# Kernel optimization log

Hardware: AMD Instinct MI355X
Metric: run time of the kernel (lower is better)

The kernel has to match this reference:

```python
import jax, jax.numpy as jnp
import numpy as np

D = 1024
H = 16
HD = D // H
DFF = 4 * D
B, L = 2, 2048
EPS = 1e-5


def setup_inputs() -> dict:
    key = jax.random.key(0)
    ks = jax.random.split(key, 12)
    s = lambda fan_in: 1.0 / np.sqrt(fan_in)
    inp = {
        "x": jax.random.normal(ks[0], (B, L, D), jnp.float32),
        "mask": jnp.ones((1, 1, L, L), jnp.bool_),
        "ln_g": jnp.ones((D,), jnp.float32),
        "ln_b": jnp.zeros((D,), jnp.float32),
        "qkv_w": jax.random.uniform(ks[1], (3 * D, D), jnp.float32, -s(D), s(D)),
        "qkv_b": jax.random.uniform(ks[2], (3 * D,), jnp.float32, -s(D), s(D)),
        "wo_w": jax.random.uniform(ks[3], (D, D), jnp.float32, -s(D), s(D)),
        "wo_b": jax.random.uniform(ks[4], (D,), jnp.float32, -s(D), s(D)),
        "m0_w": jax.random.uniform(ks[5], (DFF, D), jnp.float32, -s(D), s(D)),
        "m0_b": jax.random.uniform(ks[6], (DFF,), jnp.float32, -s(D), s(D)),
        "m1_w": jax.random.uniform(ks[7], (D, DFF), jnp.float32, -s(DFF), s(DFF)),
        "m1_b": jax.random.uniform(ks[8], (D,), jnp.float32, -s(DFF), s(DFF)),
    }
    return inp


def _layer_norm(x, g, b):
    mu = jnp.mean(x, axis=-1, keepdims=True)
    var = jnp.var(x, axis=-1, keepdims=True)
    return (x - mu) * jax.lax.rsqrt(var + EPS) * g + b


def reference(x, mask, ln_g, ln_b, qkv_w, qkv_b, wo_w, wo_b, m0_w, m0_b, m1_w, m1_b):
    b, l, d = x.shape
    # --- pre-norm self-attention ---
    xn = _layer_norm(x, ln_g, ln_b)
    qkv = xn @ qkv_w.T + qkv_b                       # [B, L, 3D]
    qkv = qkv.reshape(b, l, 3, H, HD).transpose(2, 0, 3, 1, 4)  # [3, B, H, L, HD]
    q, k, v = qkv[0], qkv[1], qkv[2]
    scores = jnp.einsum("bhld,bhmd->bhlm", q, k) / np.sqrt(HD)  # [B, H, L, L]
    scores = jnp.where(mask, scores, -1e9)
    attn = jax.nn.softmax(scores, axis=-1)
    ctx = jnp.einsum("bhlm,bhmd->bhld", attn, v)     # [B, H, L, HD]
    ctx = ctx.transpose(0, 2, 1, 3).reshape(b, l, d)
    x = x + ctx @ wo_w.T + wo_b
    # --- GELU MLP (same shared LayerNorm params) ---
    xn = _layer_norm(x, ln_g, ln_b)
    h = jax.nn.gelu(xn @ m0_w.T + m0_b, approximate=False)
    return x + h @ m1_w.T + m1_b
```

## Files before the change

kernel.cpp:

```cpp
#include <hip/hip_runtime.h>
#include <hip/hip_bf16.h>
#include <hip/hip_cooperative_groups.h>
#include <math.h>

#define BL 4096
#define DM 1024
#define NH 16
#define HD 64
#define DFF 4096
#define SEQ 2048
#define EPS 1e-5f
#define QSCALE 0.18033688011112042f

typedef __bf16 bf16x8 __attribute__((ext_vector_type(8)));
typedef float f32x4 __attribute__((ext_vector_type(4)));
typedef float f32x16 __attribute__((ext_vector_type(16)));

__device__ __forceinline__ unsigned short f2bf(float f) {
    __hip_bfloat16 h = __float2bfloat16(f);
    return *reinterpret_cast<unsigned short*>(&h);
}

__device__ __forceinline__ unsigned int pack2bf(float p0, float p1) {
    unsigned int u0 = __builtin_bit_cast(unsigned int, p0) + 0x8000u;
    unsigned int u1 = __builtin_bit_cast(unsigned int, p1) + 0x8000u;
    return __builtin_amdgcn_perm(u1, u0, 0x07060302);
}

__device__ __forceinline__ void gload_lds16(const void* g, void* l) {
    __builtin_amdgcn_global_load_lds(
        (const __attribute__((address_space(1))) unsigned int*)g,
        (__attribute__((address_space(3))) unsigned int*)l,
        16, 0, 0);
}

__global__ __launch_bounds__(256)
void prep_kernel(const float* __restrict__ x, const float* __restrict__ g,
                 const float* __restrict__ b, unsigned short* __restrict__ o,
                 const float* __restrict__ s0, const float* __restrict__ s1,
                 const float* __restrict__ s2, const float* __restrict__ s3,
                 unsigned short* __restrict__ d0, unsigned short* __restrict__ d1,
                 unsigned short* __restrict__ d2, unsigned short* __restrict__ d3,
                 int n0, int n1, int n2, int n3) {
    const int bid = blockIdx.x;
    const int tid = threadIdx.x;
    if (bid >= BL) {
        int i = (bid - BL) * 256 + tid;
        const float* s; unsigned short* d; int j = i;
        if (j < n0) { s = s0; d = d0; }
        else if ((j -= n0) < n1) { s = s1; d = d1; }
        else if ((j -= n1) < n2) { s = s2; d = d2; }
        else if ((j -= n2) < n3) { s = s3; d = d3; }
        else return;
        float4 v = ((const float4*)s)[j];
        ushort4 ov = {f2bf(v.x), f2bf(v.y), f2bf(v.z), f2bf(v.w)};
        ((ushort4*)d)[j] = ov;
        return;
    }
    const int row = bid;
    const float* xr = x + (size_t)row * DM;
    float4 v = *(const float4*)(xr + tid * 4);
    float s_  = v.x + v.y + v.z + v.w;
    float ss = v.x*v.x + v.y*v.y + v.z*v.z + v.w*v.w;
    #pragma unroll
    for (int off = 32; off > 0; off >>= 1) {
        s_ += __shfl_down(s_, off);
        ss += __shfl_down(ss, off);
    }
    __shared__ float ps[4], pss[4];
    __shared__ float sh_mu, sh_rs;
    int wid = tid >> 6, lane = tid & 63;
    if (lane == 0) { ps[wid] = s_; pss[wid] = ss; }
    __syncthreads();
    if (tid == 0) {
        float S = ps[0] + ps[1] + ps[2] + ps[3];
        float SS = pss[0] + pss[1] + pss[2] + pss[3];
        float mu = S * (1.0f / DM);
        float var = SS * (1.0f / DM) - mu * mu;
        sh_mu = mu;
        sh_rs = 1.0f / sqrtf(var + EPS);
    }
    __syncthreads();
    float mu = sh_mu, rs = sh_rs;
    float4 gv = *(const float4*)(g + tid * 4);
    float4 bv = *(const float4*)(b + tid * 4);
    ushort4 ov;
    ov.x = f2bf((v.x - mu) * rs * gv.x + bv.x);
    ov.y = f2bf((v.y - mu) * rs * gv.y + bv.y);
    ov.z = f2bf((v.z - mu) * rs * gv.z + bv.z);
    ov.w = f2bf((v.w - mu) * rs * gv.w + bv.w);
    *(ushort4*)(o + (size_t)row * DM + tid * 4) = ov;
}

template <int EPI, typename OUT_T>
__global__ __launch_bounds__(256)
void gemm_bt_mfma(const unsigned short* __restrict__ A,
                  const unsigned short* __restrict__ B,
                  const float* __restrict__ bias, const float* __restrict__ res,
                  OUT_T* __restrict__ C, int M, int N, int K,
                  unsigned short* __restrict__ vt) {
    __shared__ unsigned short smem[2][16384];
    const int tid = threadIdx.x, lane = tid & 63, wave = tid >> 6;

    const int id   = blockIdx.x;
    const int xcd  = id & 7, slot = id >> 3;
    const int R    = (M / 128) >> 3;
    const int by   = xcd * R + (slot % R);
    const int bx   = slot / R;
    const int m0 = by * 128, n0 = bx * 128;
    const int wm = (wave >> 1) * 64, wn = (wave & 1) * 64;
    const int srow = lane >> 3, sslot = lane & 7;
    const int fr = lane & 15, g = lane >> 4;

    f32x4 acc[4][4] = {};

    auto stage = [&](int b, int kt) {
        unsigned short* As = smem[b];
        unsigned short* Bs = smem[b] + 8192;
        #pragma unroll
        for (int rep = 0; rep < 8; rep++) {
            const int c = rep * 4 + wave;
            const bool isA = (c < 16);
            const int cc = isA ? c : c - 16;
            const int cr = cc * 8 + srow;
            const unsigned short* src = (isA ? A + (size_t)(m0 + cr) * K
                                             : B + (size_t)(n0 + cr) * K)
                                        + kt + ((sslot ^ (cr & 7)) * 8);
            gload_lds16(src, (char*)(isA ? As : Bs) + cc * 1024);
        }
    };

    stage(0, 0);
    const int NT = K >> 6;
    for (int ti = 0; ti < NT; ti++) {
        __syncthreads();
        if (ti + 1 < NT) stage((ti + 1) & 1, (ti + 1) * 64);
        const unsigned short* As = smem[ti & 1];
        const unsigned short* Bs = As + 8192;
        #pragma unroll
        for (int ko = 0; ko < 2; ko++) {
            const int col = (((ko * 4 + g) ^ (fr & 7)) * 8);
            bf16x8 af[4], bfv[4];
            #pragma unroll
            for (int i = 0; i < 4; i++)
                af[i] = *(const bf16x8*)(As + (wm + i * 16 + fr) * 64 + col);
            #pragma unroll
            for (int j = 0; j < 4; j++)
                bfv[j] = *(const bf16x8*)(Bs + (wn + j * 16 + fr) * 64 + col);
            #pragma unroll
            for (int i = 0; i < 4; i++)
                #pragma unroll
                for (int j = 0; j < 4; j++)
                    acc[i][j] = __builtin_amdgcn_mfma_f32_16x16x32_bf16(af[i], bfv[j], acc[i][j], 0, 0, 0);
        }
    }

    const int col  = lane & 15;
    const int rowq = (lane >> 4) * 4;
    float bs[4];
    #pragma unroll
    for (int j = 0; j < 4; j++) bs[j] = bias[n0 + wn + j * 16 + col];

    if (EPI == 3 && n0 >= 2048) {
        __syncthreads();
        unsigned short* sc = smem[0];
        #pragma unroll
        for (int i = 0; i < 4; i++) {
            const int l0 = wm + i * 16 + rowq;
            #pragma unroll
            for (int j = 0; j < 4; j++) {
                const int dcol = wn + j * 16 + col;
                float v0 = acc[i][j][0] + bs[j], v1 = acc[i][j][1] + bs[j];
                float v2 = acc[i][j][2] + bs[j], v3 = acc[i][j][3] + bs[j];
                uint2 pk = {pack2bf(v0, v1), pack2bf(v2, v3)};
                char* p = (char*)sc + dcol * 256 +
                          (((l0 >> 3) ^ (dcol & 7)) * 16) + (l0 & 7) * 2;
                *(uint2*)p = pk;
            }
        }
        __syncthreads();
        const int bb = m0 >> 11, lbase = m0 & 2047;
        #pragma unroll
        for (int k = 0; k < 8; k++) {
            const int oid = tid + k * 256;
            const int dcol = oid >> 4, lc = oid & 15;
            uint4 val = *(const uint4*)((const char*)sc + dcol * 256 +
                                        ((lc ^ (dcol & 7)) * 16));
            const int c = n0 + dcol;
            const int d = c & 63, hh2 = (c >> 6) & 15;
            *(uint4*)(vt + ((size_t)((bb * 16 + hh2) * 64 + d)) * 2048 + lbase + lc * 8) = val;
        }
        return;
    }

    #pragma unroll
    for (int i = 0; i < 4; i++) {
        #pragma unroll
        for (int r = 0; r < 4; r++) {
            const size_t row = (size_t)(m0 + wm + i * 16 + rowq + r);
            #pragma unroll
            for (int j = 0; j < 4; j++) {
                const int c = n0 + wn + j * 16 + col;
                const size_t off = row * N + c;
                float v = acc[i][j][r] + bs[j];
                if (EPI == 1) v += res[off];
                if (EPI == 2) {
                    float u = v * (0.7978845608028654f + 0.035677408136300125f * v * v);
                    float e = __builtin_amdgcn_exp2f(u * 2.885390081777927f);
                    float th = 1.0f - 2.0f * __builtin_amdgcn_rcpf(e + 1.0f);
                    v = 0.5f * v * (1.0f + th);
                }
                if (EPI == 3) {
                    float vq = (c < 1024) ? v * QSCALE : v;
                    ((unsigned short*)C)[off] = f2bf(vq);
                } else if constexpr (sizeof(OUT_T) == 2) {
                    ((unsigned short*)C)[off] = f2bf(v);
                } else {
                    ((float*)C)[off] = v;
                }
            }
        }
    }
}

template <int K>
__global__ __launch_bounds__(512)
void gemm_splitk_res(const unsigned short* __restrict__ A,
                     const unsigned short* __restrict__ B,
                     const float* __restrict__ bias,
                     const float* __restrict__ res,
                     float* __restrict__ C) {
    __shared__ unsigned short smem[2][2][16384];
    const int id   = blockIdx.x;
    const int xcd  = id & 7, slot = id >> 3;
    const int by   = xcd * 4 + (slot & 3);
    const int bx   = slot >> 2;
    const int m0 = by * 128, n0 = bx * 128;
    const int tid = threadIdx.x, lane = tid & 63, wave = tid >> 6;
    const int grp = wave >> 2, w4 = wave & 3;
    const int wm = (w4 >> 1) * 64, wn = (w4 & 1) * 64;
    const int srow = lane >> 3, sslot = lane & 7;
    const int fr = lane & 15, g = lane >> 4;
    const int kg0 = grp * (K / 2);
    constexpr int NT = K / 128;

    f32x4 acc[4][4] = {};

    auto stage = [&](int b, int kt) {
        unsigned short* As = smem[grp][b];
        unsigned short* Bs = smem[grp][b] + 8192;
        #pragma unroll
        for (int rep = 0; rep < 8; rep++) {
            const int c = rep * 4 + w4;
            const bool isA = (c < 16);
            const int cc = isA ? c : c - 16;
            const int cr = cc * 8 + srow;
            const unsigned short* src = (isA ? A + (size_t)(m0 + cr) * K
                                             : B + (size_t)(n0 + cr) * K)
                                        + kt + ((sslot ^ (cr & 7)) * 8);
            gload_lds16(src, (char*)(isA ? As : Bs) + cc * 1024);
        }
    };

    stage(0, kg0);
    for (int ti = 0; ti < NT; ti++) {
        __syncthreads();
        if (ti + 1 < NT) stage((ti + 1) & 1, kg0 + (ti + 1) * 64);
        const unsigned short* As = smem[grp][ti & 1];
        const unsigned short* Bs = As + 8192;
        #pragma unroll
        for (int ko = 0; ko < 2; ko++) {
            const int col = (((ko * 4 + g) ^ (fr & 7)) * 8);
            bf16x8 af[4], bfv[4];
            #pragma unroll
            for (int i = 0; i < 4; i++)
                af[i] = *(const bf16x8*)(As + (wm + i * 16 + fr) * 64 + col);
            #pragma unroll
            for (int j = 0; j < 4; j++)
                bfv[j] = *(const bf16x8*)(Bs + (wn + j * 16 + fr) * 64 + col);
            #pragma unroll
            for (int i = 0; i < 4; i++)
                #pragma unroll
                for (int j = 0; j < 4; j++)
                    acc[i][j] = __builtin_amdgcn_mfma_f32_16x16x32_bf16(af[i], bfv[j], acc[i][j], 0, 0, 0);
        }
    }

    __syncthreads();
    float* ox = (float*)smem;
    if (grp == 1) {
        float* bp = ox + w4 * 4096;
        #pragma unroll
        for (int i = 0; i < 4; i++)
            #pragma unroll
            for (int j = 0; j < 4; j++)
                *(f32x4*)(bp + (i * 4 + j) * 256 + lane * 4) = acc[i][j];
    }
    __syncthreads();
    if (grp == 1) return;
    {
        float* bp = ox + w4 * 4096;
        #pragma unroll
        for (int i = 0; i < 4; i++)
            #pragma unroll
            for (int j = 0; j < 4; j++)
                acc[i][j] += *(const f32x4*)(bp + (i * 4 + j) * 256 + lane * 4);
    }

    const int col = lane & 15, rowq = (lane >> 4) * 4;
    float bs[4];
    #pragma unroll
    for (int j = 0; j < 4; j++) bs[j] = bias[n0 + wn + j * 16 + col];
    #pragma unroll
    for (int i = 0; i < 4; i++)
        #pragma unroll
        for (int r = 0; r < 4; r++) {
            const size_t row = (size_t)(m0 + wm + i * 16 + rowq + r);
            #pragma unroll
            for (int j = 0; j < 4; j++) {
                const int c = n0 + wn + j * 16 + col;
                const size_t off = row * 1024 + c;
                C[off] = acc[i][j][r] + bs[j] + res[off];
            }
        }
}

__global__ __launch_bounds__(512)
void fused_wo_ln(const unsigned short* __restrict__ A,
                 const unsigned short* __restrict__ B,
                 const float* __restrict__ bias,
                 const float* __restrict__ res,
                 float* __restrict__ C,
                 const float* __restrict__ gw,
                 const float* __restrict__ bw,
                 unsigned short* __restrict__ xn) {
    constexpr int K = 1024;
    __shared__ unsigned short smem[2][2][16384];
    const int id   = blockIdx.x;
    const int xcd  = id & 7, slot = id >> 3;
    const int by   = xcd * 4 + (slot & 3);
    const int bx   = slot >> 2;
    const int m0 = by * 128, n0 = bx * 128;
    const int tid = threadIdx.x, lane = tid & 63, wave = tid >> 6;
    const int grp = wave >> 2, w4 = wave & 3;
    const int wm = (w4 >> 1) * 64, wn = (w4 & 1) * 64;
    const int srow = lane >> 3, sslot = lane & 7;
    const int fr = lane & 15, g = lane >> 4;
    const int kg0 = grp * (K / 2);
    constexpr int NT = K / 128;

    f32x4 acc[4][4] = {};

    auto stage = [&](int b, int kt) {
        unsigned short* As = smem[grp][b];
        unsigned short* Bs = smem[grp][b] + 8192;
        #pragma unroll
        for (int rep = 0; rep < 8; rep++) {
            const int c = rep * 4 + w4;
            const bool isA = (c < 16);
            const int cc = isA ? c : c - 16;
            const int cr = cc * 8 + srow;
            const unsigned short* src = (isA ? A + (size_t)(m0 + cr) * K
                                             : B + (size_t)(n0 + cr) * K)
                                        + kt + ((sslot ^ (cr & 7)) * 8);
            gload_lds16(src, (char*)(isA ? As : Bs) + cc * 1024);
        }
    };

    stage(0, kg0);
    for (int ti = 0; ti < NT; ti++) {
        __syncthreads();
        if (ti + 1 < NT) stage((ti + 1) & 1, kg0 + (ti + 1) * 64);
        const unsigned short* As = smem[grp][ti & 1];
        const unsigned short* Bs = As + 8192;
        #pragma unroll
        for (int ko = 0; ko < 2; ko++) {
            const int col = (((ko * 4 + g) ^ (fr & 7)) * 8);
            bf16x8 af[4], bfv[4];
            #pragma unroll
            for (int i = 0; i < 4; i++)
                af[i] = *(const bf16x8*)(As + (wm + i * 16 + fr) * 64 + col);
            #pragma unroll
            for (int j = 0; j < 4; j++)
                bfv[j] = *(const bf16x8*)(Bs + (wn + j * 16 + fr) * 64 + col);
            #pragma unroll
            for (int i = 0; i < 4; i++)
                #pragma unroll
                for (int j = 0; j < 4; j++)
                    acc[i][j] = __builtin_amdgcn_mfma_f32_16x16x32_bf16(af[i], bfv[j], acc[i][j], 0, 0, 0);
        }
    }

    __syncthreads();
    float* ox = (float*)smem;
    if (grp == 1) {
        float* bp = ox + w4 * 4096;
        #pragma unroll
        for (int i = 0; i < 4; i++)
            #pragma unroll
            for (int j = 0; j < 4; j++)
                *(f32x4*)(bp + (i * 4 + j) * 256 + lane * 4) = acc[i][j];
    }
    __syncthreads();
    if (grp == 0) {
        float* bp = ox + w4 * 4096;
        #pragma unroll
        for (int i = 0; i < 4; i++)
            #pragma unroll
            for (int j = 0; j < 4; j++)
                acc[i][j] += *(const f32x4*)(bp + (i * 4 + j) * 256 + lane * 4);

        const int col = lane & 15, rowq = (lane >> 4) * 4;
        float bs[4];
        #pragma unroll
        for (int j = 0; j < 4; j++) bs[j] = bias[n0 + wn + j * 16 + col];
        #pragma unroll
        for (int i = 0; i < 4; i++)
            #pragma unroll
            for (int r = 0; r < 4; r++) {
                const size_t row = (size_t)(m0 + wm + i * 16 + rowq + r);
                #pragma unroll
                for (int j = 0; j < 4; j++) {
                    const int c = n0 + wn + j * 16 + col;
                    const size_t off = row * 1024 + c;
                    C[off] = acc[i][j][r] + bs[j] + res[off];
                }
            }
    }

    cooperative_groups::this_grid().sync();

    float* ph = (float*)smem;
    const int team = tid >> 8, tt = tid & 255;
    const int wl = (tid >> 6) & 3;
    for (int it = 0; it < 8; it++) {
        const int row = id * 16 + it * 2 + team;
        const float* xr = C + (size_t)row * DM;
        float4 v = *(const float4*)(xr + tt * 4);
        float s  = v.x + v.y + v.z + v.w;
        float ss = v.x*v.x + v.y*v.y + v.z*v.z + v.w*v.w;
        #pragma unroll
        for (int off = 32; off > 0; off >>= 1) {
            s  += __shfl_down(s, off);
            ss += __shfl_down(ss, off);
        }
        if ((tid & 63) == 0) { ph[team * 8 + wl] = s; ph[team * 8 + 4 + wl] = ss; }
        __syncthreads();
        float S  = ph[team*8+0] + ph[team*8+1] + ph[team*8+2] + ph[team*8+3];
        float SS = ph[team*8+4] + ph[team*8+5] + ph[team*8+6] + ph[team*8+7];
        float mu = S * (1.0f / DM);
        float var = SS * (1.0f / DM) - mu * mu;
        float rs = 1.0f / sqrtf(var + EPS);
        float4 gv = *(const float4*)(gw + tt * 4);
        float4 bv = *(const float4*)(bw + tt * 4);
        ushort4 ov;
        ov.x = f2bf((v.x - mu) * rs * gv.x + bv.x);
        ov.y = f2bf((v.y - mu) * rs * gv.y + bv.y);
        ov.z = f2bf((v.z - mu) * rs * gv.z + bv.z);
        ov.w = f2bf((v.w - mu) * rs * gv.w + bv.w);
        *(ushort4*)(xn + (size_t)row * DM + tt * 4) = ov;
        __syncthreads();
    }
}

__global__ __launch_bounds__(512)
void attn_mfma(const unsigned short* __restrict__ qkv,
               const unsigned short* __restrict__ vt,
               unsigned short* __restrict__ ctx) {
    __shared__ unsigned short smem[2][16384];
    const int bid = blockIdx.x;
    const int xcd = bid & 7, sl = bid >> 3;
    const int qt = sl & 15, pg = sl >> 4;
    const int pair = pg * 8 + xcd;
    const int h = pair & 15, b = pair >> 4;
    const int tid = threadIdx.x, lane = tid & 63, wave = tid >> 6;
    const int grp = wave >> 2, w4 = wave & 3;
    const int hh = lane >> 5, mm = lane & 31;
    const int q0 = b * 2048 + qt * 128 + w4 * 32;

    unsigned short* Ks = smem[grp];
    unsigned short* Vt = smem[grp] + 8192;

    bf16x8 qf[4];
    const unsigned short* qb = qkv + (size_t)(q0 + mm) * 3072 + h * 64 + hh * 8;
    #pragma unroll
    for (int s = 0; s < 4; s++) qf[s] = *(const bf16x8*)(qb + s * 16);

    const int skey = lane >> 3;
    const int sgr  = (lane & 7) ^ (skey & 7);
    const unsigned short* kbase = qkv + ((size_t)(b * 2048) + skey) * 3072 + 1024 + h * 64 + sgr * 8;
    const unsigned short* vbase = vt + ((size_t)((b * 16 + h) * 64) + skey) * 2048 + sgr * 8;

    float l_lane = 0.0f;
    f32x16 o_acc[2] = {};
    const int kt0 = grp * 1024;

    for (int ti = 0; ti < 8; ti++) {
        const int kt = kt0 + ti * 128;
        __syncthreads();
        #pragma unroll
        for (int rep = 0; rep < 4; rep++) {
            int c = rep * 4 + w4;
            gload_lds16(kbase + (size_t)(kt + c * 8) * 3072, (char*)Ks + c * 1024);
        }
        #pragma unroll
        for (int rep = 0; rep < 2; rep++) {
            int c = rep * 4 + w4;
            gload_lds16(vbase + (size_t)(c * 8) * 2048 + kt,      (char*)Vt + c * 1024);
            gload_lds16(vbase + (size_t)(c * 8) * 2048 + kt + 64, (char*)Vt + 8192 + c * 1024);
        }
        __syncthreads();

        #pragma unroll
        for (int sub = 0; sub < 2; sub++) {
            f32x16 sT[2] = {};
            __builtin_amdgcn_s_setprio(1);
            #pragma unroll
            for (int t = 0; t < 2; t++)
                #pragma unroll
                for (int s = 0; s < 4; s++) {
                    bf16x8 kf = *(const bf16x8*)(Ks + (sub * 64 + t * 32 + mm) * 64 + ((s * 2 + hh) ^ (mm & 7)) * 8);
                    sT[t] = __builtin_amdgcn_mfma_f32_32x32x16_bf16(kf, qf[s], sT[t], 0, 0, 0);
                }
            __builtin_amdgcn_s_setprio(0);

            unsigned int pk[2][8];
            #pragma unroll
            for (int t = 0; t < 2; t++)
                #pragma unroll
                for (int e = 0; e < 8; e++) {
                    float p0 = __builtin_amdgcn_exp2f(sT[t][2 * e]);
                    float p1 = __builtin_amdgcn_exp2f(sT[t][2 * e + 1]);
                    l_lane += p0 + p1;
                    pk[t][e] = pack2bf(p0, p1);
                }

            __builtin_amdgcn_s_setprio(1);
            #pragma unroll
            for (int w = 0; w < 4; w++) {
                const int t = w >> 1, eb = (w & 1) * 4;
                unsigned int a0 = pk[t][eb + 0], a1 = pk[t][eb + 1];
                unsigned int a2 = pk[t][eb + 2], a3 = pk[t][eb + 3];
                asm("v_permlane32_swap_b32 %0, %1" : "+v"(a0), "+v"(a2));
                asm("v_permlane32_swap_b32 %0, %1" : "+v"(a1), "+v"(a3));
                union { unsigned int u[4]; bf16x8 v; } af;
                af.u[0] = a0; af.u[1] = a1; af.u[2] = a2; af.u[3] = a3;
                #pragma unroll
                for (int dt = 0; dt < 2; dt++) {
                    bf16x8 vf = *(const bf16x8*)(Vt + sub * 4096 + (dt * 32 + mm) * 64 + ((w * 2 + hh) ^ (mm & 7)) * 8);
                    o_acc[dt] = __builtin_amdgcn_mfma_f32_32x32x16_bf16(af.v, vf, o_acc[dt], 0, 0, 0);
                }
            }
            __builtin_amdgcn_s_setprio(0);
        }
    }

    float l_red = l_lane + __shfl_xor(l_lane, 32);
    __syncthreads();
    float* ox = (float*)smem;
    float* lx = (float*)((char*)smem + 32768);
    if (grp == 1) {
        float* base = ox + w4 * 2048;
        #pragma unroll
        for (int dt = 0; dt < 2; dt++)
            #pragma unroll
            for (int r = 0; r < 16; r++)
                base[(dt * 16 + r) * 64 + lane] = o_acc[dt][r];
        if (hh == 0) lx[w4 * 32 + mm] = l_red;
    }
    __syncthreads();
    if (grp == 1) return;
    {
        float* base = ox + w4 * 2048;
        #pragma unroll
        for (int dt = 0; dt < 2; dt++)
            #pragma unroll
            for (int r = 0; r < 16; r++)
                o_acc[dt][r] += base[(dt * 16 + r) * 64 + lane];
        l_red += lx[w4 * 32 + mm];
    }

    float inv_own = 1.0f / l_red;
    #pragma unroll
    for (int r = 0; r < 16; r++) {
        const int rowq = (r & 3) + 8 * (r >> 2) + 4 * hh;
        float inv = __shfl(inv_own, rowq);
        size_t base = (size_t)(q0 + rowq) * 1024 + h * 64 + mm;
        ctx[base]      = f2bf(o_acc[0][r] * inv);
        ctx[base + 32] = f2bf(o_acc[1][r] * inv);
    }
}

extern "C" void kernel_launch(void* const* d_in, const int* in_sizes, int n_in,
                              void* d_out, int out_size, void* d_ws, size_t ws_size,
                              hipStream_t stream) {
    const float* x     = (const float*)d_in[0];
    const float* ln_g  = (const float*)d_in[2];
    const float* ln_b  = (const float*)d_in[3];
    const float* qkv_w = (const float*)d_in[4];
    const float* qkv_b = (const float*)d_in[5];
    const float* wo_w  = (const float*)d_in[6];
    const float* wo_b  = (const float*)d_in[7];
    const float* m0_w  = (const float*)d_in[8];
    const float* m0_b  = (const float*)d_in[9];
    const float* m1_w  = (const float*)d_in[10];
    const float* m1_b  = (const float*)d_in[11];
    float* out = (float*)d_out;

    char* ws = (char*)d_ws;
    unsigned short* xn_bf  = (unsigned short*)(ws);
    unsigned short* qkv_bf = (unsigned short*)(ws + (size_t)8  * 1024 * 1024);
    unsigned short* vt_bf  = (unsigned short*)(ws + (size_t)32 * 1024 * 1024);
    unsigned short* ctx_bf = (unsigned short*)(ws + (size_t)40 * 1024 * 1024);
    unsigned short* h_bf   = (unsigned short*)(ws + (size_t)48 * 1024 * 1024);
    unsigned short* qkvw_b = (unsigned short*)(ws + (size_t)80 * 1024 * 1024);
    unsigned short* wow_b  = (unsigned short*)(ws + (size_t)86 * 1024 * 1024);
    unsigned short* m0w_b  = (unsigned short*)(ws + (size_t)88 * 1024 * 1024);
    unsigned short* m1w_b  = (unsigned short*)(ws + (size_t)96 * 1024 * 1024);

    {
        int n0 = 3 * DM * DM / 4, n1 = DM * DM / 4, n2 = DFF * DM / 4, n3 = DM * DFF / 4;
        int tot = n0 + n1 + n2 + n3;
        prep_kernel<<<BL + (tot + 255) / 256, 256, 0, stream>>>(
            x, ln_g, ln_b, xn_bf,
            qkv_w, wo_w, m0_w, m1_w, qkvw_b, wow_b, m0w_b, m1w_b, n0, n1, n2, n3);
    }

    gemm_bt_mfma<3, unsigned short><<<(3072 / 128) * (BL / 128), 256, 0, stream>>>(
        xn_bf, qkvw_b, qkv_b, nullptr, qkv_bf, BL, 3072, DM, vt_bf);
    attn_mfma<<<2 * NH * (SEQ / 128), 512, 0, stream>>>(qkv_bf, vt_bf, ctx_bf);
    {
        void* args[] = {(void*)&ctx_bf, (void*)&wow_b, (void*)&wo_b, (void*)&x,
                        (void*)&out, (void*)&ln_g, (void*)&ln_b, (void*)&xn_bf};
        hipLaunchCooperativeKernel((void*)fused_wo_ln, dim3(256), dim3(512),
                                   args, 0, stream);
    }
    gemm_bt_mfma<2, unsigned short><<<(DFF / 128) * (BL / 128), 256, 0, stream>>>(
        xn_bf, m0w_b, m0_b, nullptr, h_bf, BL, DFF, DM, nullptr);
    gemm_splitk_res<4096><<<256, 512, 0, stream>>>(h_bf, m1w_b, m1_b, out, out);
}
```

Measured before the change: 379.0 us.

## Replace cooperative grid sync with per-row-block atomic counter for fused LayerNorm

Drops the cooperative launch and grid-wide barrier in the Wo GEMM plus LayerNorm kernel. Each 128-row block now increments a counter once its output tile is written, and the last of the 8 column tiles to finish runs LayerNorm on those 128 rows, one wave per row. This avoids the whole-grid wait and the cooperative launch overhead, at the cost of leaving the LayerNorm work on 32 blocks only. Counters are zeroed in the prep kernel, and a fallback path with a separate GEMM and LN kernel is used if the workspace is too small.

```diff
diff --git a/kernel.cpp b/kernel.cpp
--- a/kernel.cpp
+++ b/kernel.cpp
@@ -1,6 +1,5 @@
 #include <hip/hip_runtime.h>
 #include <hip/hip_bf16.h>
-#include <hip/hip_cooperative_groups.h>
 #include <math.h>
 
 #define BL 4096
@@ -41,10 +40,11 @@
                  const float* __restrict__ s2, const float* __restrict__ s3,
                  unsigned short* __restrict__ d0, unsigned short* __restrict__ d1,
                  unsigned short* __restrict__ d2, unsigned short* __restrict__ d3,
-                 int n0, int n1, int n2, int n3) {
+                 int n0, int n1, int n2, int n3, unsigned int* cntp) {
     const int bid = blockIdx.x;
     const int tid = threadIdx.x;
     if (bid >= BL) {
+        if (cntp && bid == BL && tid < 32) cntp[tid] = 0;
         int i = (bid - BL) * 256 + tid;
         const float* s; unsigned short* d; int j = i;
         if (j < n0) { s = s0; d = d0; }
@@ -71,6 +71,45 @@
     __shared__ float sh_mu, sh_rs;
     int wid = tid >> 6, lane = tid & 63;
     if (lane == 0) { ps[wid] = s_; pss[wid] = ss; }
+    __syncthreads();
+    if (tid == 0) {
+        float S = ps[0] + ps[1] + ps[2] + ps[3];
+        float SS = pss[0] + pss[1] + pss[2] + pss[3];
+        float mu = S * (1.0f / DM);
+        float var = SS * (1.0f / DM) - mu * mu;
+        sh_mu = mu;
+        sh_rs = 1.0f / sqrtf(var + EPS);
+    }
+    __syncthreads();
+    float mu = sh_mu, rs = sh_rs;
+    float4 gv = *(const float4*)(g + tid * 4);
+    float4 bv = *(const float4*)(b + tid * 4);
+    ushort4 ov;
+    ov.x = f2bf((v.x - mu) * rs * gv.x + bv.x);
+    ov.y = f2bf((v.y - mu) * rs * gv.y + bv.y);
+    ov.z = f2bf((v.z - mu) * rs * gv.z + bv.z);
+    ov.w = f2bf((v.w - mu) * rs * gv.w + bv.w);
+    *(ushort4*)(o + (size_t)row * DM + tid * 4) = ov;
+}
+
+__global__ __launch_bounds__(256)
+void ln_kernel(const float* __restrict__ x, const float* __restrict__ g,
+               const float* __restrict__ b, unsigned short* __restrict__ o) {
+    int row = blockIdx.x;
+    int tid = threadIdx.x;
+    const float* xr = x + (size_t)row * DM;
+    float4 v = *(const float4*)(xr + tid * 4);
+    float s  = v.x + v.y + v.z + v.w;
+    float ss = v.x*v.x + v.y*v.y + v.z*v.z + v.w*v.w;
+    #pragma unroll
+    for (int off = 32; off > 0; off >>= 1) {
+        s  += __shfl_down(s, off);
+        ss += __shfl_down(ss, off);
+    }
+    __shared__ float ps[4], pss[4];
+    __shared__ float sh_mu, sh_rs;
+    int wid = tid >> 6, lane = tid & 63;
+    if (lane == 0) { ps[wid] = s; pss[wid] = ss; }
     __syncthreads();
     if (tid == 0) {
         float S = ps[0] + ps[1] + ps[2] + ps[3];
@@ -326,14 +365,15 @@
 }
 
 __global__ __launch_bounds__(512)
-void fused_wo_ln(const unsigned short* __restrict__ A,
-                 const unsigned short* __restrict__ B,
-                 const float* __restrict__ bias,
-                 const float* __restrict__ res,
-                 float* __restrict__ C,
-                 const float* __restrict__ gw,
-                 const float* __restrict__ bw,
-                 unsigned short* __restrict__ xn) {
+void gemm_wo_ln(const unsigned short* __restrict__ A,
+                const unsigned short* __restrict__ B,
+                const float* __restrict__ bias,
+                const float* __restrict__ res,
+                float* __restrict__ C,
+                const float* __restrict__ gw,
+                const float* __restrict__ bw,
+                unsigned short* __restrict__ xn,
+                unsigned int* __restrict__ cnt) {
     constexpr int K = 1024;
     __shared__ unsigned short smem[2][2][16384];
     const int id   = blockIdx.x;
@@ -428,38 +468,50 @@
             }
     }
 
-    cooperative_groups::this_grid().sync();
-
-    float* ph = (float*)smem;
-    const int team = tid >> 8, tt = tid & 255;
-    const int wl = (tid >> 6) & 3;
-    for (int it = 0; it < 8; it++) {
-        const int row = id * 16 + it * 2 + team;
-        const float* xr = C + (size_t)row * DM;
-        float4 v = *(const float4*)(xr + tt * 4);
-        float s  = v.x + v.y + v.z + v.w;
-        float ss = v.x*v.x + v.y*v.y + v.z*v.z + v.w*v.w;
+    __syncthreads();
+    unsigned int* flag = (unsigned int*)smem;
+    if (tid == 0) {
+        __threadfence();
+        flag[0] = atomicAdd(&cnt[by], 1u);
+    }
+    __syncthreads();
+    if (flag[0] != 7) return;
+    __threadfence();
+
+    float4 gv[4], bv[4];
+    #pragma unroll
+    for (int c = 0; c < 4; c++) {
+        gv[c] = *(const float4*)(gw + c * 256 + lane * 4);
+        bv[c] = *(const float4*)(bw + c * 256 + lane * 4);
+    }
+    for (int it = 0; it < 16; it++) {
+        const int row = m0 + it * 8 + wave;
+        const float* cr = C + (size_t)row * DM;
+        float4 v[4]; float s = 0.0f, ss = 0.0f;
+        #pragma unroll
+        for (int c = 0; c < 4; c++) {
+            v[c] = *(const float4*)(cr + c * 256 + lane * 4);
+            s  += v[c].x + v[c].y + v[c].z + v[c].w;
+            ss += v[c].x*v[c].x + v[c].y*v[c].y + v[c].z*v[c].z + v[c].w*v[c].w;
+        }
         #pragma unroll
         for (int off = 32; off > 0; off >>= 1) {
             s  += __shfl_down(s, off);
             ss += __shfl_down(ss, off);
         }
-        if ((tid & 63) == 0) { ph[team * 8 + wl] = s; ph[team * 8 + 4 + wl] = ss; }
-        __syncthreads();
-        float S  = ph[team*8+0] + ph[team*8+1] + ph[team*8+2] + ph[team*8+3];
-        float SS = ph[team*8+4] + ph[team*8+5] + ph[team*8+6] + ph[team*8+7];
-        float mu = S * (1.0f / DM);
-        float var = SS * (1.0f / DM) - mu * mu;
-        float rs = 1.0f / sqrtf(var + EPS);
-        float4 gv = *(const float4*)(gw + tt * 4);
-        float4 bv = *(const float4*)(bw + tt * 4);
-        ushort4 ov;
-        ov.x = f2bf((v.x - mu) * rs * gv.x + bv.x);
-        ov.y = f2bf((v.y - mu) * rs * gv.y + bv.y);
-        ov.z = f2bf((v.z - mu) * rs * gv.z + bv.z);
-        ov.w = f2bf((v.w - mu) * rs * gv.w + bv.w);
-        *(ushort4*)(xn + (size_t)row * DM + tt * 4) = ov;
-        __syncthreads();
+        s = __shfl(s, 0); ss = __shfl(ss, 0);
+        const float mu = s * (1.0f / DM);
+        const float rs = 1.0f / sqrtf(ss * (1.0f / DM) - mu * mu + EPS);
+        unsigned short* xr = xn + (size_t)row * DM;
+        #pragma unroll
+        for (int c = 0; c < 4; c++) {
+            ushort4 ov;
+            ov.x = f2bf((v[c].x - mu) * rs * gv[c].x + bv[c].x);
+            ov.y = f2bf((v[c].y - mu) * rs * gv[c].y + bv[c].y);
+            ov.z = f2bf((v[c].z - mu) * rs * gv[c].z + bv[c].z);
+            ov.w = f2bf((v[c].w - mu) * rs * gv[c].w + bv[c].w);
+            *(ushort4*)(xr + c * 256 + lane * 4) = ov;
+        }
     }
 }
 
@@ -617,23 +669,28 @@
     unsigned short* wow_b  = (unsigned short*)(ws + (size_t)86 * 1024 * 1024);
     unsigned short* m0w_b  = (unsigned short*)(ws + (size_t)88 * 1024 * 1024);
     unsigned short* m1w_b  = (unsigned short*)(ws + (size_t)96 * 1024 * 1024);
+    const bool fuse_ln = ws_size >= (size_t)104 * 1024 * 1024 + 4096;
+    unsigned int* cnt = fuse_ln ? (unsigned int*)(ws + (size_t)104 * 1024 * 1024)
+                                : nullptr;
 
     {
         int n0 = 3 * DM * DM / 4, n1 = DM * DM / 4, n2 = DFF * DM / 4, n3 = DM * DFF / 4;
         int tot = n0 + n1 + n2 + n3;
         prep_kernel<<<BL + (tot + 255) / 256, 256, 0, stream>>>(
             x, ln_g, ln_b, xn_bf,
-            qkv_w, wo_w, m0_w, m1_w, qkvw_b, wow_b, m0w_b, m1w_b, n0, n1, n2, n3);
+            qkv_w, wo_w, m0_w, m1_w, qkvw_b, wow_b, m0w_b, m1w_b,
+            n0, n1, n2, n3, cnt);
     }
 
     gemm_bt_mfma<3, unsigned short><<<(3072 / 128) * (BL / 128), 256, 0, stream>>>(
         xn_bf, qkvw_b, qkv_b, nullptr, qkv_bf, BL, 3072, DM, vt_bf);
     attn_mfma<<<2 * NH * (SEQ / 128), 512, 0, stream>>>(qkv_bf, vt_bf, ctx_bf);
-    {
-        void* args[] = {(void*)&ctx_bf, (void*)&wow_b, (void*)&wo_b, (void*)&x,
-                        (void*)&out, (void*)&ln_g, (void*)&ln_b, (void*)&xn_bf};
-        hipLaunchCooperativeKernel((void*)fused_wo_ln, dim3(256), dim3(512),
-                                   args, 0, stream);
+    if (fuse_ln) {
+        gemm_wo_ln<<<256, 512, 0, stream>>>(
+            ctx_bf, wow_b, wo_b, x, out, ln_g, ln_b, xn_bf, cnt);
+    } else {
+        gemm_splitk_res<1024><<<256, 512, 0, stream>>>(ctx_bf, wow_b, wo_b, x, out);
+        ln_kernel<<<BL, 256, 0, stream>>>(out, ln_g, ln_b, xn_bf);
     }
     gemm_bt_mfma<2, unsigned short><<<(DFF / 128) * (BL / 128), 256, 0, stream>>>(
         xn_bf, m0w_b, m0_b, nullptr, h_bf, BL, DFF, DM, nullptr);
```

New measurement: 334.0 us. 11.9% less time.
